# Performance work log

Measured on AMD Instinct MI355X. Metric: run time of the kernel, lower is better.

## Reference

```python
import jax, jax.numpy as jnp
import numpy as np

EMB, HID, NH = 512, 256, 8
DH = HID // NH
LN_EPS = 1e-5


def _mk(key, shape, scale=0.02):
    return jax.random.normal(key, shape, dtype=jnp.float32) * scale


def setup_inputs() -> dict:
    key = jax.random.key(0)
    ks = jax.random.split(key, 24)
    B, S = 8, 256
    return {
        "memory_embeddings": jax.random.normal(ks[0], (B, S, EMB), dtype=jnp.float32),
        # memory_encoder: Linear(512,256) -> LayerNorm -> ReLU -> Linear(256,256)
        "enc_w1": _mk(ks[1], (HID, EMB)), "enc_b1": jnp.zeros((HID,), jnp.float32),
        "ln_g": jnp.ones((HID,), jnp.float32), "ln_b": jnp.zeros((HID,), jnp.float32),
        "enc_w2": _mk(ks[2], (HID, HID)), "enc_b2": jnp.zeros((HID,), jnp.float32),
        # MultiheadAttention packed qkv + out proj
        "in_proj_w": _mk(ks[3], (3 * HID, HID)), "in_proj_b": jnp.zeros((3 * HID,), jnp.float32),
        "out_w": _mk(ks[4], (HID, HID)), "out_b": jnp.zeros((HID,), jnp.float32),
        # consistency head: Linear(256,128) -> ReLU -> Linear(128,1) -> Sigmoid
        "cons_w1": _mk(ks[5], (HID // 2, HID)), "cons_b1": jnp.zeros((HID // 2,), jnp.float32),
        "cons_w2": _mk(ks[6], (1, HID // 2)), "cons_b2": jnp.zeros((1,), jnp.float32),
        # hallucination detector
        "hall_w1": _mk(ks[7], (HID // 2, HID)), "hall_b1": jnp.zeros((HID // 2,), jnp.float32),
        "hall_w2": _mk(ks[8], (1, HID // 2)), "hall_b2": jnp.zeros((1,), jnp.float32),
        # contradiction analyzer: Linear(512,256) -> ReLU -> Linear(256,1) -> Sigmoid
        "con_w1": _mk(ks[9], (HID, 2 * HID)), "con_b1": jnp.zeros((HID,), jnp.float32),
        "con_w2": _mk(ks[10], (1, HID)), "con_b2": jnp.zeros((1,), jnp.float32),
    }


def _forward(memory_embeddings, enc_w1, enc_b1, ln_g, ln_b, enc_w2, enc_b2,
             in_proj_w, in_proj_b, out_w, out_b,
             cons_w1, cons_b1, cons_w2, cons_b2,
             hall_w1, hall_b1, hall_w2, hall_b2,
             con_w1, con_b1, con_w2, con_b2):
    B, S, _ = memory_embeddings.shape
    # --- memory encoder (dropout in eval mode = identity) ---
    h = memory_embeddings @ enc_w1.T + enc_b1                      # [B,S,HID]
    mu = h.mean(-1, keepdims=True)
    var = ((h - mu) ** 2).mean(-1, keepdims=True)
    h = (h - mu) * jax.lax.rsqrt(var + LN_EPS) * ln_g + ln_b
    mf = jax.nn.relu(h) @ enc_w2.T + enc_b2                        # [B,S,HID]
    # --- multihead self-attention (batch_first, averaged attn weights) ---
    qkv = mf @ in_proj_w.T + in_proj_b                              # [B,S,3H]
    q, k, v = jnp.split(qkv, 3, axis=-1)
    def heads(t):  # [B,S,H] -> [B,NH,S,DH]
        return t.reshape(B, S, NH, DH).transpose(0, 2, 1, 3)
    q, k, v = heads(q), heads(k), heads(v)
    scores = jnp.einsum('bhsd,bhtd->bhst', q, k) / jnp.sqrt(jnp.float32(DH))
    attn = jax.nn.softmax(scores, axis=-1)                          # [B,NH,S,S]
    ctx = jnp.einsum('bhst,bhtd->bhsd', attn, v)
    ctx = ctx.transpose(0, 2, 1, 3).reshape(B, S, HID)
    attended = ctx @ out_w.T + out_b                                # [B,S,HID]
    attn_weights = attn.mean(axis=1)                                # [B,S,S]
    # --- pooled heads ---
    pooled = attended.mean(axis=1)                                  # [B,HID]
    cons = jax.nn.sigmoid(jax.nn.relu(pooled @ cons_w1.T + cons_b1) @ cons_w2.T + cons_b2)[:, 0]
    hall = jax.nn.sigmoid(jax.nn.relu(pooled @ hall_w1.T + hall_b1) @ hall_w2.T + hall_b2)[:, 0]
    # --- contradiction matrix over all i<j pairs (vectorized gather/MLP/scatter) ---
    iu, ju = np.triu_indices(S, k=1)                                # static indices
    Wa, Wb = con_w1[:, :HID], con_w1[:, HID:]                       # split concat-linear
    a = mf @ Wa.T                                                   # [B,S,HID]
    b = mf @ Wb.T
    hid = jax.nn.relu(a[:, iu] + b[:, ju] + con_b1)                 # [B,P,HID]
    sc = jax.nn.sigmoid(hid @ con_w2.T + con_b2)[..., 0]            # [B,P]
    M = jnp.zeros((B, S, S), dtype=mf.dtype)
    M = M.at[:, iu, ju].set(sc)
    M = M.at[:, ju, iu].set(sc)
    return cons, hall, M, attn_weights


def reference(memory_embeddings, enc_w1, enc_b1, ln_g, ln_b, enc_w2, enc_b2,
              in_proj_w, in_proj_b, out_w, out_b,
              cons_w1, cons_b1, cons_w2, cons_b2,
              hall_w1, hall_b1, hall_w2, hall_b2,
              con_w1, con_b1, con_w2, con_b2):
    return _forward(memory_embeddings, enc_w1, enc_b1, ln_g, ln_b, enc_w2, enc_b2,
                    in_proj_w, in_proj_b, out_w, out_b,
                    cons_w1, cons_b1, cons_w2, cons_b2,
                    hall_w1, hall_b1, hall_w2, hall_b2,
                    con_w1, con_b1, con_w2, con_b2)
```

## Files before the change

### kernel.cpp

```cpp
#include <hip/hip_runtime.h>
#include <math.h>

typedef __attribute__((ext_vector_type(8))) short bf16x8;
typedef __attribute__((ext_vector_type(4))) float f32x4;

__device__ __forceinline__ short f2b(float f) {
  union { float f; unsigned u; } v; v.f = f;
  unsigned u = v.u + 0x7fffu + ((v.u >> 16) & 1u);
  return (short)(u >> 16);
}

__device__ __forceinline__ bf16x8 cvt8(float4 a, float4 b) {
  bf16x8 r;
  r[0] = f2b(a.x); r[1] = f2b(a.y); r[2] = f2b(a.z); r[3] = f2b(a.w);
  r[4] = f2b(b.x); r[5] = f2b(b.y); r[6] = f2b(b.z); r[7] = f2b(b.w);
  return r;
}

__global__ __launch_bounds__(512) void k_enc(
    const float* __restrict__ me,
    const float* __restrict__ w1f, const float* __restrict__ b1,
    const float* __restrict__ g, const float* __restrict__ lb,
    const float* __restrict__ w2f, const float* __restrict__ b2,
    unsigned short* __restrict__ mfb, float* __restrict__ poolctx) {
  __shared__ float hh[16 * 260];
  __shared__ unsigned short rA[16 * 264];
  __shared__ unsigned short mfs[16 * 256];
  int tid = threadIdx.x, lane = tid & 63, w = tid >> 6;
  int row0 = blockIdx.x * 16;
  int m = lane & 15, q = lane >> 4;
  if (blockIdx.x == 0) {
    float4 z = {0.f, 0.f, 0.f, 0.f};
    ((float4*)poolctx)[tid] = z;
  }
  {
    f32x4 acc0 = (f32x4){0.f, 0.f, 0.f, 0.f};
    f32x4 acc1 = (f32x4){0.f, 0.f, 0.f, 0.f};
    const float* ap = me + (size_t)(row0 + m) * 512 + q * 8;
    const float* bp0 = w1f + (size_t)(w * 32 + m) * 512 + q * 8;
    const float* bp1 = w1f + (size_t)(w * 32 + 16 + m) * 512 + q * 8;
    float4 pa[4][2], pb[4][2][2];
#pragma unroll
    for (int d = 0; d < 4; ++d) {
      pa[d][0] = *(const float4*)(ap + d * 32);
      pa[d][1] = *(const float4*)(ap + d * 32 + 4);
      pb[d][0][0] = *(const float4*)(bp0 + d * 32);
      pb[d][0][1] = *(const float4*)(bp0 + d * 32 + 4);
      pb[d][1][0] = *(const float4*)(bp1 + d * 32);
      pb[d][1][1] = *(const float4*)(bp1 + d * 32 + 4);
    }
#pragma unroll
    for (int it = 0; it < 16; ++it) {
      int slot = it & 3;
      float4 a0 = pa[slot][0], a1 = pa[slot][1];
      float4 b00 = pb[slot][0][0], b01 = pb[slot][0][1];
      float4 b10 = pb[slot][1][0], b11 = pb[slot][1][1];
      if (it + 4 < 16) {
        pa[slot][0] = *(const float4*)(ap + (it + 4) * 32);
        pa[slot][1] = *(const float4*)(ap + (it + 4) * 32 + 4);
        pb[slot][0][0] = *(const float4*)(bp0 + (it + 4) * 32);
        pb[slot][0][1] = *(const float4*)(bp0 + (it + 4) * 32 + 4);
        pb[slot][1][0] = *(const float4*)(bp1 + (it + 4) * 32);
        pb[slot][1][1] = *(const float4*)(bp1 + (it + 4) * 32 + 4);
      }
      bf16x8 af = cvt8(a0, a1);
      acc0 = __builtin_amdgcn_mfma_f32_16x16x32_bf16(af, cvt8(b00, b01), acc0, 0, 0, 0);
      acc1 = __builtin_amdgcn_mfma_f32_16x16x32_bf16(af, cvt8(b10, b11), acc1, 0, 0, 0);
    }
#pragma unroll
    for (int nt = 0; nt < 2; ++nt) {
      int col = w * 32 + nt * 16 + m;
      float bias = b1[col];
      f32x4 a = nt ? acc1 : acc0;
#pragma unroll
      for (int reg = 0; reg < 4; ++reg)
        hh[(q * 4 + reg) * 260 + col] = a[reg] + bias;
    }
  }
  __syncthreads();
  {
    float4 g4 = *(const float4*)(g + lane * 4);
    float4 lb4 = *(const float4*)(lb + lane * 4);
#pragma unroll
    for (int rr = 0; rr < 2; ++rr) {
      int r = w * 2 + rr;
      float4 v = *(const float4*)&hh[r * 260 + lane * 4];
      float s1 = v.x + v.y + v.z + v.w;
      float s2 = v.x * v.x + v.y * v.y + v.z * v.z + v.w * v.w;
#pragma unroll
      for (int o = 32; o > 0; o >>= 1) {
        s1 += __shfl_xor(s1, o, 64);
        s2 += __shfl_xor(s2, o, 64);
      }
      float mu = s1 * (1.f / 256.f);
      float var = s2 * (1.f / 256.f) - mu * mu;
      float rs = rsqrtf(var + 1e-5f);
      unsigned short y0 = (unsigned short)f2b(fmaxf((v.x - mu) * rs * g4.x + lb4.x, 0.f));
      unsigned short y1 = (unsigned short)f2b(fmaxf((v.y - mu) * rs * g4.y + lb4.y, 0.f));
      unsigned short y2 = (unsigned short)f2b(fmaxf((v.z - mu) * rs * g4.z + lb4.z, 0.f));
      unsigned short y3 = (unsigned short)f2b(fmaxf((v.w - mu) * rs * g4.w + lb4.w, 0.f));
      uint2 pk;
      pk.x = (unsigned)y0 | ((unsigned)y1 << 16);
      pk.y = (unsigned)y2 | ((unsigned)y3 << 16);
      *(uint2*)&rA[r * 264 + lane * 4] = pk;
    }
  }
  __syncthreads();
  {
    f32x4 acc0 = (f32x4){0.f, 0.f, 0.f, 0.f};
    f32x4 acc1 = (f32x4){0.f, 0.f, 0.f, 0.f};
    const float* cp0 = w2f + (size_t)(w * 32 + m) * 256 + q * 8;
    const float* cp1 = w2f + (size_t)(w * 32 + 16 + m) * 256 + q * 8;
    float4 pb[4][2][2];
#pragma unroll
    for (int d = 0; d < 4; ++d) {
      pb[d][0][0] = *(const float4*)(cp0 + d * 32);
      pb[d][0][1] = *(const float4*)(cp0 + d * 32 + 4);
      pb[d][1][0] = *(const float4*)(cp1 + d * 32);
      pb[d][1][1] = *(const float4*)(cp1 + d * 32 + 4);
    }
#pragma unroll
    for (int it = 0; it < 8; ++it) {
      int slot = it & 3;
      float4 b00 = pb[slot][0][0], b01 = pb[slot][0][1];
      float4 b10 = pb[slot][1][0], b11 = pb[slot][1][1];
      if (it + 4 < 8) {
        pb[slot][0][0] = *(const float4*)(cp0 + (it + 4) * 32);
        pb[slot][0][1] = *(const float4*)(cp0 + (it + 4) * 32 + 4);
        pb[slot][1][0] = *(const float4*)(cp1 + (it + 4) * 32);
        pb[slot][1][1] = *(const float4*)(cp1 + (it + 4) * 32 + 4);
      }
      bf16x8 af = *(const bf16x8*)&rA[m * 264 + it * 32 + q * 8];
      acc0 = __builtin_amdgcn_mfma_f32_16x16x32_bf16(af, cvt8(b00, b01), acc0, 0, 0, 0);
      acc1 = __builtin_amdgcn_mfma_f32_16x16x32_bf16(af, cvt8(b10, b11), acc1, 0, 0, 0);
    }
#pragma unroll
    for (int nt = 0; nt < 2; ++nt) {
      int col = w * 32 + nt * 16 + m;
      float bias = b2[col];
      f32x4 a = nt ? acc1 : acc0;
#pragma unroll
      for (int reg = 0; reg < 4; ++reg)
        mfs[(q * 4 + reg) * 256 + col] = (unsigned short)f2b(a[reg] + bias);
    }
  }
  __syncthreads();
  {
    const uint4* src = (const uint4*)mfs;
    uint4* dst = (uint4*)(mfb + (size_t)row0 * 256);
    dst[tid] = src[tid];
  }
}

__global__ __launch_bounds__(256) void k_proj5(
    const unsigned short* __restrict__ mfb,
    const float* __restrict__ wq, const float* __restrict__ wc,
    const float* __restrict__ bq, const float* __restrict__ cb1,
    float* __restrict__ qkv, float* __restrict__ amat,
    float* __restrict__ bmat) {
  int tid = threadIdx.x, lane = tid & 63, w = tid >> 6;
  int row0 = blockIdx.x * 16;
  int part = blockIdx.y;
  int m = lane & 15, q = lane >> 4;
  const float* Wbase;
  size_t wstride;
  if (part < 3) { Wbase = wq + (size_t)part * 256 * 256; wstride = 256; }
  else { Wbase = wc + (part == 4 ? 256 : 0); wstride = 512; }
  bf16x8 a[8];
#pragma unroll
  for (int ks = 0; ks < 8; ++ks)
    a[ks] = *(const bf16x8*)(mfb + (size_t)(row0 + m) * 256 + ks * 32 + q * 8);
  f32x4 acc[4];
#pragma unroll
  for (int i = 0; i < 4; ++i) acc[i] = (f32x4){0.f, 0.f, 0.f, 0.f};
  const float* bp[4];
#pragma unroll
  for (int nt = 0; nt < 4; ++nt)
    bp[nt] = Wbase + (size_t)(w * 64 + nt * 16 + m) * wstride + q * 8;
  float4 pb[4][4][2];
#pragma unroll
  for (int d = 0; d < 4; ++d)
#pragma unroll
    for (int nt = 0; nt < 4; ++nt) {
      pb[d][nt][0] = *(const float4*)(bp[nt] + d * 32);
      pb[d][nt][1] = *(const float4*)(bp[nt] + d * 32 + 4);
    }
#pragma unroll
  for (int it = 0; it < 8; ++it) {
    int slot = it & 3;
    float4 b0l = pb[slot][0][0], b0h = pb[slot][0][1];
    float4 b1l = pb[slot][1][0], b1h = pb[slot][1][1];
    float4 b2l = pb[slot][2][0], b2h = pb[slot][2][1];
    float4 b3l = pb[slot][3][0], b3h = pb[slot][3][1];
    if (it + 4 < 8) {
#pragma unroll
      for (int nt = 0; nt < 4; ++nt) {
        pb[slot][nt][0] = *(const float4*)(bp[nt] + (it + 4) * 32);
        pb[slot][nt][1] = *(const float4*)(bp[nt] + (it + 4) * 32 + 4);
      }
    }
    acc[0] = __builtin_amdgcn_mfma_f32_16x16x32_bf16(a[it], cvt8(b0l, b0h), acc[0], 0, 0, 0);
    acc[1] = __builtin_amdgcn_mfma_f32_16x16x32_bf16(a[it], cvt8(b1l, b1h), acc[1], 0, 0, 0);
    acc[2] = __builtin_amdgcn_mfma_f32_16x16x32_bf16(a[it], cvt8(b2l, b2h), acc[2], 0, 0, 0);
    acc[3] = __builtin_amdgcn_mfma_f32_16x16x32_bf16(a[it], cvt8(b3l, b3h), acc[3], 0, 0, 0);
  }
#pragma unroll
  for (int nt = 0; nt < 4; ++nt) {
    int col = w * 64 + nt * 16 + m;
    float bias;
    float* dst;
    int ld;
    if (part < 3) { bias = bq[part * 256 + col]; dst = qkv + part * 256; ld = 768; }
    else if (part == 3) { bias = cb1[col]; dst = amat; ld = 256; }
    else { bias = 0.f; dst = bmat; ld = 256; }
#pragma unroll
    for (int reg = 0; reg < 4; ++reg) {
      int row = row0 + q * 4 + reg;
      dst[(size_t)row * ld + col] = acc[nt][reg] + bias;
    }
  }
}

__global__ __launch_bounds__(256) void k_attn_fused(
    const float* __restrict__ qkv, unsigned short* __restrict__ attnb,
    float* __restrict__ poolctx) {
  __shared__ float qs[32 * 32];
  __shared__ unsigned short ps[32 * 264];
  __shared__ unsigned short vt[32 * 264];
  int blk = blockIdx.x;
  int sg = blk & 7, bh = blk >> 3, h = bh & 7, b = bh >> 3;
  int tid = threadIdx.x, lane = tid & 63, w = tid >> 6;
  {
    int r = tid >> 3, c4 = tid & 7;
    float4 v = *(const float4*)(qkv + ((size_t)(b * 256 + sg * 32 + r)) * 768 + h * 32 + c4 * 4);
    *(float4*)&qs[r * 32 + c4 * 4] = v;
  }
  {
    const float4* vr = (const float4*)(qkv + ((size_t)(b * 256 + tid)) * 768 + 512 + h * 32);
#pragma unroll
    for (int d4 = 0; d4 < 8; ++d4) {
      float4 vv = vr[d4];
      vt[(d4 * 4 + 0) * 264 + tid] = (unsigned short)f2b(vv.x);
      vt[(d4 * 4 + 1) * 264 + tid] = (unsigned short)f2b(vv.y);
      vt[(d4 * 4 + 2) * 264 + tid] = (unsigned short)f2b(vv.z);
      vt[(d4 * 4 + 3) * 264 + tid] = (unsigned short)f2b(vv.w);
    }
  }
  __syncthreads();
  int r0 = w * 8;
  float sc[8][4];
#pragma unroll
  for (int r = 0; r < 8; ++r)
#pragma unroll
    for (int tt = 0; tt < 4; ++tt) sc[r][tt] = 0.f;
#pragma unroll
  for (int tt = 0; tt < 4; ++tt) {
    int t = tt * 64 + lane;
    const float4* kp = (const float4*)(qkv + ((size_t)(b * 256 + t)) * 768 + 256 + h * 32);
#pragma unroll
    for (int d4 = 0; d4 < 8; ++d4) {
      float4 kv = kp[d4];
#pragma unroll
      for (int r = 0; r < 8; ++r) {
        float4 qv = *(const float4*)&qs[(r0 + r) * 32 + d4 * 4];
        sc[r][tt] += qv.x * kv.x + qv.y * kv.y + qv.z * kv.z + qv.w * kv.w;
      }
    }
  }
  const float scale = 0.17677669529663689f;
  for (int r = 0; r < 8; ++r) {
    float v0 = sc[r][0] * scale, v1 = sc[r][1] * scale;
    float v2 = sc[r][2] * scale, v3 = sc[r][3] * scale;
    float mx = fmaxf(fmaxf(v0, v1), fmaxf(v2, v3));
#pragma unroll
    for (int o = 32; o > 0; o >>= 1) mx = fmaxf(mx, __shfl_xor(mx, o, 64));
    float e0 = expf(v0 - mx), e1 = expf(v1 - mx), e2 = expf(v2 - mx), e3 = expf(v3 - mx);
    float s = e0 + e1 + e2 + e3;
#pragma unroll
    for (int o = 32; o > 0; o >>= 1) s += __shfl_xor(s, o, 64);
    float inv = 1.f / s;
    unsigned short* prow = ps + (r0 + r) * 264;
    prow[lane] = (unsigned short)f2b(e0 * inv);
    prow[64 + lane] = (unsigned short)f2b(e1 * inv);
    prow[128 + lane] = (unsigned short)f2b(e2 * inv);
    prow[192 + lane] = (unsigned short)f2b(e3 * inv);
  }
  __syncthreads();
  {
    int r = tid >> 3, seg = tid & 7;
    const uint4* src = (const uint4*)&ps[r * 264 + seg * 32];
    uint4* dst = (uint4*)(attnb + ((size_t)(bh * 256 + sg * 32 + r)) * 256 + seg * 32);
    dst[0] = src[0]; dst[1] = src[1]; dst[2] = src[2]; dst[3] = src[3];
  }
  {
    int mt = w & 1, dt = w >> 1;
    int mm = lane & 15, qq = lane >> 4;
    f32x4 a = (f32x4){0.f, 0.f, 0.f, 0.f};
#pragma unroll
    for (int ks = 0; ks < 256; ks += 32) {
      bf16x8 af = *(const bf16x8*)&ps[(mt * 16 + mm) * 264 + ks + qq * 8];
      bf16x8 bf = *(const bf16x8*)&vt[(dt * 16 + mm) * 264 + ks + qq * 8];
      a = __builtin_amdgcn_mfma_f32_16x16x32_bf16(af, bf, a, 0, 0, 0);
    }
    float colsum = a[0] + a[1] + a[2] + a[3];
    colsum += __shfl_xor(colsum, 16, 64);
    colsum += __shfl_xor(colsum, 32, 64);
    if (lane < 16)
      atomicAdd(&poolctx[b * 256 + h * 32 + dt * 16 + mm], colsum);
  }
}

__global__ __launch_bounds__(256) void k_tail(
    const float* __restrict__ amat, const float* __restrict__ bmat,
    const float* __restrict__ conw2, const float* __restrict__ conb2,
    float* __restrict__ M,
    const unsigned short* __restrict__ attnb, float* __restrict__ out_aw,
    const float* __restrict__ poolctx,
    const float* __restrict__ outw, const float* __restrict__ outb,
    const float* __restrict__ cw1, const float* __restrict__ cb1h,
    const float* __restrict__ cw2, const float* __restrict__ cb2,
    const float* __restrict__ hw1, const float* __restrict__ hb1,
    const float* __restrict__ hw2, const float* __restrict__ hb2,
    float* __restrict__ out) {
  __shared__ float smem[32 * 132 * 2 + 256];
  int bx = blockIdx.x, tid = threadIdx.x;
  if (bx < 288) {
    float* As = smem;
    float* Bs = smem + 32 * 132;
    float* w2s = smem + 32 * 132 * 2;
    int b = bx / 36, tix = bx % 36;
    int it = 0, rem = tix;
    while (rem >= 8 - it) { rem -= 8 - it; ++it; }
    int jt = it + rem;
    int tj = tid & 15, ti = tid >> 4;
    w2s[tid] = conw2[tid];
    float acc00 = 0, acc01 = 0, acc10 = 0, acc11 = 0;
    const float* Ab = amat + ((size_t)(b * 256 + it * 32)) * 256;
    const float* Bb = bmat + ((size_t)(b * 256 + jt * 32)) * 256;
    for (int ch = 0; ch < 2; ++ch) {
      __syncthreads();
#pragma unroll
      for (int k = 0; k < 4; ++k) {
        int f = tid + k * 256;
        int r = f >> 5, c4 = f & 31;
        float4 va = *(const float4*)(Ab + (size_t)r * 256 + ch * 128 + c4 * 4);
        float4 vb = *(const float4*)(Bb + (size_t)r * 256 + ch * 128 + c4 * 4);
        *(float4*)&As[r * 132 + c4 * 4] = va;
        *(float4*)&Bs[r * 132 + c4 * 4] = vb;
      }
      __syncthreads();
      const float* a0 = As + (2 * ti) * 132;
      const float* a1 = a0 + 132;
      const float* b0 = Bs + (2 * tj) * 132;
      const float* b1 = b0 + 132;
      const float* w2c = w2s + ch * 128;
      for (int d = 0; d < 128; d += 4) {
        float4 wv = *(const float4*)&w2c[d];
        float4 av0 = *(const float4*)&a0[d];
        float4 av1 = *(const float4*)&a1[d];
        float4 bv0 = *(const float4*)&b0[d];
        float4 bv1 = *(const float4*)&b1[d];
        acc00 += fmaxf(av0.x + bv0.x, 0.f) * wv.x + fmaxf(av0.y + bv0.y, 0.f) * wv.y
               + fmaxf(av0.z + bv0.z, 0.f) * wv.z + fmaxf(av0.w + bv0.w, 0.f) * wv.w;
        acc01 += fmaxf(av0.x + bv1.x, 0.f) * wv.x + fmaxf(av0.y + bv1.y, 0.f) * wv.y
               + fmaxf(av0.z + bv1.z, 0.f) * wv.z + fmaxf(av0.w + bv1.w, 0.f) * wv.w;
        acc10 += fmaxf(av1.x + bv0.x, 0.f) * wv.x + fmaxf(av1.y + bv0.y, 0.f) * wv.y
               + fmaxf(av1.z + bv0.z, 0.f) * wv.z + fmaxf(av1.w + bv0.w, 0.f) * wv.w;
        acc11 += fmaxf(av1.x + bv1.x, 0.f) * wv.x + fmaxf(av1.y + bv1.y, 0.f) * wv.y
               + fmaxf(av1.z + bv1.z, 0.f) * wv.z + fmaxf(av1.w + bv1.w, 0.f) * wv.w;
      }
    }
    float c2 = conb2[0];
    float s00 = 1.f / (1.f + expf(-(acc00 + c2)));
    float s01 = 1.f / (1.f + expf(-(acc01 + c2)));
    float s10 = 1.f / (1.f + expf(-(acc10 + c2)));
    float s11 = 1.f / (1.f + expf(-(acc11 + c2)));
    float* Mb = M + ((size_t)b << 16);
    int i0 = it * 32 + 2 * ti, i1 = i0 + 1;
    int j0 = jt * 32 + 2 * tj, j1 = j0 + 1;
    if (it != jt) {
      Mb[i0 * 256 + j0] = s00; Mb[j0 * 256 + i0] = s00;
      Mb[i0 * 256 + j1] = s01; Mb[j1 * 256 + i0] = s01;
      Mb[i1 * 256 + j0] = s10; Mb[j0 * 256 + i1] = s10;
      Mb[i1 * 256 + j1] = s11; Mb[j1 * 256 + i1] = s11;
    } else {
      if (j0 > i0) { Mb[i0 * 256 + j0] = s00; Mb[j0 * 256 + i0] = s00; }
      else if (j0 == i0) Mb[i0 * 256 + j0] = 0.f;
      if (j1 > i0) { Mb[i0 * 256 + j1] = s01; Mb[j1 * 256 + i0] = s01; }
      if (j0 > i1) { Mb[i1 * 256 + j0] = s10; Mb[j0 * 256 + i1] = s10; }
      if (j1 > i1) { Mb[i1 * 256 + j1] = s11; Mb[j1 * 256 + i1] = s11; }
      else if (j1 == i1) Mb[i1 * 256 + j1] = 0.f;
    }
  } else if (bx < 544) {
    int gid = (bx - 288) * 256 + tid;
    int b = gid >> 13, e8 = gid & 8191;
    size_t e = (size_t)e8 * 8;
    float s0 = 0, s1 = 0, s2 = 0, s3 = 0, s4 = 0, s5 = 0, s6 = 0, s7 = 0;
#pragma unroll
    for (int h = 0; h < 8; ++h) {
      uint4 v = *(const uint4*)(attnb + (((size_t)(b * 8 + h)) << 16) + e);
      s0 += __uint_as_float(v.x << 16); s1 += __uint_as_float(v.x & 0xffff0000u);
      s2 += __uint_as_float(v.y << 16); s3 += __uint_as_float(v.y & 0xffff0000u);
      s4 += __uint_as_float(v.z << 16); s5 += __uint_as_float(v.z & 0xffff0000u);
      s6 += __uint_as_float(v.w << 16); s7 += __uint_as_float(v.w & 0xffff0000u);
    }
    float* dst = out_aw + ((size_t)b << 16) + e;
    float4 r0 = {s0 * 0.125f, s1 * 0.125f, s2 * 0.125f, s3 * 0.125f};
    float4 r1 = {s4 * 0.125f, s5 * 0.125f, s6 * 0.125f, s7 * 0.125f};
    *(float4*)dst = r0;
    *(float4*)(dst + 4) = r1;
  } else {
    float* pc = smem;
    float* psh = smem + 256;
    float* red = smem + 512;
    int b = bx - 544, j = tid;
    pc[j] = poolctx[b * 256 + j] * (1.f / 256.f);
    __syncthreads();
    float s = outb[j];
    const float4* wr = (const float4*)(outw + (size_t)j * 256);
    for (int k4 = 0; k4 < 64; ++k4) {
      float4 wv = wr[k4];
      const float* p = pc + k4 * 4;
      s += p[0] * wv.x + p[1] * wv.y + p[2] * wv.z + p[3] * wv.w;
    }
    psh[j] = s;
    __syncthreads();
    int jj = j & 127;
    bool isH = j >= 128;
    const float* w1 = isH ? hw1 : cw1;
    const float* bb1 = isH ? hb1 : cb1h;
    const float* w2 = isH ? hw2 : cw2;
    float a = bb1[jj];
    const float4* w1r = (const float4*)(w1 + (size_t)jj * 256);
    for (int k4 = 0; k4 < 64; ++k4) {
      float4 wv = w1r[k4];
      const float* p = psh + k4 * 4;
      a += p[0] * wv.x + p[1] * wv.y + p[2] * wv.z + p[3] * wv.w;
    }
    float v = fmaxf(a, 0.f) * w2[jj];
#pragma unroll
    for (int o = 32; o > 0; o >>= 1) v += __shfl_xor(v, o, 64);
    if ((j & 63) == 0) red[j >> 6] = v;
    __syncthreads();
    if (j == 0) {
      float c = red[0] + red[1] + cb2[0];
      float h = red[2] + red[3] + hb2[0];
      out[b] = 1.f / (1.f + expf(-c));
      out[8 + b] = 1.f / (1.f + expf(-h));
    }
  }
}

extern "C" void kernel_launch(void* const* d_in, const int* in_sizes, int n_in,
                              void* d_out, int out_size, void* d_ws, size_t ws_size,
                              hipStream_t stream) {
  const float* me        = (const float*)d_in[0];
  const float* enc_w1    = (const float*)d_in[1];
  const float* enc_b1    = (const float*)d_in[2];
  const float* ln_g      = (const float*)d_in[3];
  const float* ln_b      = (const float*)d_in[4];
  const float* enc_w2    = (const float*)d_in[5];
  const float* enc_b2    = (const float*)d_in[6];
  const float* in_proj_w = (const float*)d_in[7];
  const float* in_proj_b = (const float*)d_in[8];
  const float* out_w     = (const float*)d_in[9];
  const float* out_b     = (const float*)d_in[10];
  const float* cons_w1   = (const float*)d_in[11];
  const float* cons_b1   = (const float*)d_in[12];
  const float* cons_w2   = (const float*)d_in[13];
  const float* cons_b2   = (const float*)d_in[14];
  const float* hall_w1   = (const float*)d_in[15];
  const float* hall_b1   = (const float*)d_in[16];
  const float* hall_w2   = (const float*)d_in[17];
  const float* hall_b2   = (const float*)d_in[18];
  const float* con_w1    = (const float*)d_in[19];
  const float* con_b1    = (const float*)d_in[20];
  const float* con_w2    = (const float*)d_in[21];
  const float* con_b2    = (const float*)d_in[22];

  float* ws = (float*)d_ws;
  float* qkv  = ws;
  unsigned short* attnb = (unsigned short*)(ws + 1572864);
  float* amat = ws + 3670016;
  float* bmat = ws + 4194304;
  unsigned short* mfb = (unsigned short*)(ws + 4718592);
  float* poolctx = ws + 4980736;

  float* out    = (float*)d_out;
  float* out_M  = out + 16;
  float* out_aw = out + 16 + 524288;

  k_enc<<<128, 512, 0, stream>>>(me, enc_w1, enc_b1, ln_g, ln_b,
                                 enc_w2, enc_b2, mfb, poolctx);
  k_proj5<<<dim3(128, 5), 256, 0, stream>>>(mfb, in_proj_w, con_w1,
                                            in_proj_b, con_b1,
                                            qkv, amat, bmat);
  k_attn_fused<<<512, 256, 0, stream>>>(qkv, attnb, poolctx);
  k_tail<<<552, 256, 0, stream>>>(amat, bmat, con_w2, con_b2, out_M,
                                  attnb, out_aw, poolctx,
                                  out_w, out_b,
                                  cons_w1, cons_b1, cons_w2, cons_b2,
                                  hall_w1, hall_b1, hall_w2, hall_b2, out);
}
```

Before: 211.2 us.

## Compute attention scores with bf16 MFMA and cross-wave softmax reduction

Replaces the scalar fp32 Q·K^T score loop in the attention kernel with bf16 MFMA tiles. Q and K are staged into padded LDS as bf16. Softmax row max and sum are now reduced across two waves through small shared arrays with extra barriers, and expf is replaced by __expf. This cuts the FMA count and the repeated global K loads, at the cost of bf16 rounding on Q and K scores, more LDS use, and two more barriers.

Measured after the change: 194.1 us. 1.09x faster.

```diff
diff --git a/kernel.cpp b/kernel.cpp
--- a/kernel.cpp
+++ b/kernel.cpp
@@ -221,19 +221,34 @@
   }
 }
 
-__global__ __launch_bounds__(256) void k_attn_fused(
+__global__ __launch_bounds__(256) void k_attn_mfma(
     const float* __restrict__ qkv, unsigned short* __restrict__ attnb,
     float* __restrict__ poolctx) {
-  __shared__ float qs[32 * 32];
+  __shared__ unsigned short qs[32 * 40];
+  __shared__ unsigned short kb[256 * 40];
+  __shared__ unsigned short vt[32 * 264];
   __shared__ unsigned short ps[32 * 264];
-  __shared__ unsigned short vt[32 * 264];
+  __shared__ float redm[2][32];
+  __shared__ float reds[2][32];
   int blk = blockIdx.x;
   int sg = blk & 7, bh = blk >> 3, h = bh & 7, b = bh >> 3;
   int tid = threadIdx.x, lane = tid & 63, w = tid >> 6;
+  int m = lane & 15, q = lane >> 4;
   {
     int r = tid >> 3, c4 = tid & 7;
     float4 v = *(const float4*)(qkv + ((size_t)(b * 256 + sg * 32 + r)) * 768 + h * 32 + c4 * 4);
-    *(float4*)&qs[r * 32 + c4 * 4] = v;
+    unsigned short* dst = &qs[r * 40 + c4 * 4];
+    dst[0] = (unsigned short)f2b(v.x); dst[1] = (unsigned short)f2b(v.y);
+    dst[2] = (unsigned short)f2b(v.z); dst[3] = (unsigned short)f2b(v.w);
+  }
+#pragma unroll
+  for (int i = 0; i < 8; ++i) {
+    int f = i * 256 + tid;
+    int r = f >> 3, c4 = f & 7;
+    float4 v = *(const float4*)(qkv + ((size_t)(b * 256 + r)) * 768 + 256 + h * 32 + c4 * 4);
+    unsigned short* dst = &kb[r * 40 + c4 * 4];
+    dst[0] = (unsigned short)f2b(v.x); dst[1] = (unsigned short)f2b(v.y);
+    dst[2] = (unsigned short)f2b(v.z); dst[3] = (unsigned short)f2b(v.w);
   }
   {
     const float4* vr = (const float4*)(qkv + ((size_t)(b * 256 + tid)) * 768 + 512 + h * 32);
@@ -247,43 +262,68 @@
     }
   }
   __syncthreads();
-  int r0 = w * 8;
-  float sc[8][4];
-#pragma unroll
-  for (int r = 0; r < 8; ++r)
-#pragma unroll
-    for (int tt = 0; tt < 4; ++tt) sc[r][tt] = 0.f;
-#pragma unroll
-  for (int tt = 0; tt < 4; ++tt) {
-    int t = tt * 64 + lane;
-    const float4* kp = (const float4*)(qkv + ((size_t)(b * 256 + t)) * 768 + 256 + h * 32);
-#pragma unroll
-    for (int d4 = 0; d4 < 8; ++d4) {
-      float4 kv = kp[d4];
-#pragma unroll
-      for (int r = 0; r < 8; ++r) {
-        float4 qv = *(const float4*)&qs[(r0 + r) * 32 + d4 * 4];
-        sc[r][tt] += qv.x * kv.x + qv.y * kv.y + qv.z * kv.z + qv.w * kv.w;
-      }
+  int mt = w & 1, ng = w >> 1;
+  int lrow = mt * 16 + q * 4;
+  f32x4 acc[8];
+  {
+    bf16x8 af = *(const bf16x8*)&qs[(mt * 16 + m) * 40 + q * 8];
+#pragma unroll
+    for (int nt = 0; nt < 8; ++nt) {
+      bf16x8 bf = *(const bf16x8*)&kb[(ng * 128 + nt * 16 + m) * 40 + q * 8];
+      acc[nt] = __builtin_amdgcn_mfma_f32_16x16x32_bf16(
+          af, bf, (f32x4){0.f, 0.f, 0.f, 0.f}, 0, 0, 0);
     }
   }
   const float scale = 0.17677669529663689f;
-  for (int r = 0; r < 8; ++r) {
-    float v0 = sc[r][0] * scale, v1 = sc[r][1] * scale;
-    float v2 = sc[r][2] * scale, v3 = sc[r][3] * scale;
-    float mx = fmaxf(fmaxf(v0, v1), fmaxf(v2, v3));
-#pragma unroll
-    for (int o = 32; o > 0; o >>= 1) mx = fmaxf(mx, __shfl_xor(mx, o, 64));
-    float e0 = expf(v0 - mx), e1 = expf(v1 - mx), e2 = expf(v2 - mx), e3 = expf(v3 - mx);
-    float s = e0 + e1 + e2 + e3;
-#pragma unroll
-    for (int o = 32; o > 0; o >>= 1) s += __shfl_xor(s, o, 64);
-    float inv = 1.f / s;
-    unsigned short* prow = ps + (r0 + r) * 264;
-    prow[lane] = (unsigned short)f2b(e0 * inv);
-    prow[64 + lane] = (unsigned short)f2b(e1 * inv);
-    prow[128 + lane] = (unsigned short)f2b(e2 * inv);
-    prow[192 + lane] = (unsigned short)f2b(e3 * inv);
+#pragma unroll
+  for (int nt = 0; nt < 8; ++nt)
+#pragma unroll
+    for (int reg = 0; reg < 4; ++reg) acc[nt][reg] *= scale;
+  float pm[4];
+#pragma unroll
+  for (int reg = 0; reg < 4; ++reg) {
+    float mx = acc[0][reg];
+#pragma unroll
+    for (int nt = 1; nt < 8; ++nt) mx = fmaxf(mx, acc[nt][reg]);
+#pragma unroll
+    for (int o = 1; o < 16; o <<= 1) mx = fmaxf(mx, __shfl_xor(mx, o, 64));
+    pm[reg] = mx;
+  }
+  if (m == 0) {
+#pragma unroll
+    for (int reg = 0; reg < 4; ++reg) redm[ng][lrow + reg] = pm[reg];
+  }
+  __syncthreads();
+  float inv[4];
+  float psum[4];
+#pragma unroll
+  for (int reg = 0; reg < 4; ++reg) {
+    float Mv = fmaxf(redm[0][lrow + reg], redm[1][lrow + reg]);
+    float s = 0.f;
+#pragma unroll
+    for (int nt = 0; nt < 8; ++nt) {
+      float e = __expf(acc[nt][reg] - Mv);
+      acc[nt][reg] = e;
+      s += e;
+    }
+#pragma unroll
+    for (int o = 1; o < 16; o <<= 1) s += __shfl_xor(s, o, 64);
+    psum[reg] = s;
+  }
+  if (m == 0) {
+#pragma unroll
+    for (int reg = 0; reg < 4; ++reg) reds[ng][lrow + reg] = psum[reg];
+  }
+  __syncthreads();
+#pragma unroll
+  for (int reg = 0; reg < 4; ++reg)
+    inv[reg] = 1.f / (reds[0][lrow + reg] + reds[1][lrow + reg]);
+#pragma unroll
+  for (int nt = 0; nt < 8; ++nt) {
+    int t = ng * 128 + nt * 16 + m;
+#pragma unroll
+    for (int reg = 0; reg < 4; ++reg)
+      ps[(lrow + reg) * 264 + t] = (unsigned short)f2b(acc[nt][reg] * inv[reg]);
   }
   __syncthreads();
   {
@@ -293,20 +333,19 @@
     dst[0] = src[0]; dst[1] = src[1]; dst[2] = src[2]; dst[3] = src[3];
   }
   {
-    int mt = w & 1, dt = w >> 1;
-    int mm = lane & 15, qq = lane >> 4;
+    int dt = w >> 1;
     f32x4 a = (f32x4){0.f, 0.f, 0.f, 0.f};
 #pragma unroll
     for (int ks = 0; ks < 256; ks += 32) {
-      bf16x8 af = *(const bf16x8*)&ps[(mt * 16 + mm) * 264 + ks + qq * 8];
-      bf16x8 bf = *(const bf16x8*)&vt[(dt * 16 + mm) * 264 + ks + qq * 8];
+      bf16x8 af = *(const bf16x8*)&ps[(mt * 16 + m) * 264 + ks + q * 8];
+      bf16x8 bf = *(const bf16x8*)&vt[(dt * 16 + m) * 264 + ks + q * 8];
       a = __builtin_amdgcn_mfma_f32_16x16x32_bf16(af, bf, a, 0, 0, 0);
     }
     float colsum = a[0] + a[1] + a[2] + a[3];
     colsum += __shfl_xor(colsum, 16, 64);
     colsum += __shfl_xor(colsum, 32, 64);
     if (lane < 16)
-      atomicAdd(&poolctx[b * 256 + h * 32 + dt * 16 + mm], colsum);
+      atomicAdd(&poolctx[b * 256 + h * 32 + dt * 16 + m], colsum);
   }
 }
 
@@ -495,7 +534,7 @@
   k_proj5<<<dim3(128, 5), 256, 0, stream>>>(mfb, in_proj_w, con_w1,
                                             in_proj_b, con_b1,
                                             qkv, amat, bmat);
-  k_attn_fused<<<512, 256, 0, stream>>>(qkv, attnb, poolctx);
+  k_attn_mfma<<<512, 256, 0, stream>>>(qkv, attnb, poolctx);
   k_tail<<<552, 256, 0, stream>>>(amat, bmat, con_w2, con_b2, out_M,
                                   attnb, out_aw, poolctx,
                                   out_w, out_b,
```
